# Optimization experiments

Hardware: AMD Instinct MI355X
Metric: run time of the kernel (lower is better)

The kernel has to match this reference:

```python
import jax, jax.numpy as jnp
import numpy as np

H = 8          # heads
D_MODEL = 64   # padded embedding dim (power of 2)
D_K = 8        # per-head dim -> NQ=3 qubits
SEQ = 32
NQ = 3
DIM2 = D_K * D_K  # 2*NQ qubit joint space
W_MUL = float(np.sqrt(2.0) * 5 ** (-0.5))  # PQC he_std * lrmul

# ---- static circuit unitaries (qubit 0 = most significant / leftmost in kron) ----

def _cnot(n, c, t):
    dim = 2 ** n
    P = np.zeros((dim, dim), np.complex64)
    for b in range(dim):
        if (b >> (n - 1 - c)) & 1:
            P[b ^ (1 << (n - 1 - t)), b] = 1.0
        else:
            P[b, b] = 1.0
    return P

def _cnot_ring(n):
    U = np.eye(2 ** n, dtype=np.complex64)
    for t in range(n):
        U = _cnot(n, t, (t + 1) % n) @ U  # later gates multiply on the left
    return U

UC6 = jnp.asarray(_cnot_ring(2 * NQ))  # (64,64) entangling ring used by score + sum circuits
MZ6 = jnp.asarray(((-1.0) ** np.array([bin(i).count('1') for i in range(2 ** (2 * NQ))])).astype(np.complex64))  # Z^{otimes 2n} diagonal

# ---- parameterized single-qubit rotations (batched, differentiable) ----

def _rx(t):
    c = jnp.cos(t / 2).astype(jnp.complex64)
    s = jnp.sin(t / 2).astype(jnp.complex64)
    return jnp.stack([jnp.stack([c, -1j * s], -1), jnp.stack([-1j * s, c], -1)], -2)

def _ry(t):
    c = jnp.cos(t / 2).astype(jnp.complex64)
    s = jnp.sin(t / 2).astype(jnp.complex64)
    return jnp.stack([jnp.stack([c, -s], -1), jnp.stack([s, c], -1)], -2)

def _rz(t):
    e = jnp.exp(-0.5j * t.astype(jnp.complex64))
    z = jnp.zeros_like(e)
    return jnp.stack([jnp.stack([e, z], -1), jnp.stack([z, e.conj()], -1)], -2)

def _kron3(a, b, c):
    out = jnp.einsum('...ad,...be,...cf->...abcdef', a, b, c)
    return out.reshape(out.shape[:-6] + (D_K, D_K))

def _pqc_unitaries(w):
    # w: (H, 3, NQ*3); per qubit apply rx, ry, rz -> per-qubit u = Rz@Ry@Rx, circuit = kron
    a = (w * W_MUL).reshape(H, 3, NQ, 3)
    u = _rz(a[..., 2]) @ _ry(a[..., 1]) @ _rx(a[..., 0])  # (H,3,NQ,2,2)
    return _kron3(u[..., 0, :, :], u[..., 1, :, :], u[..., 2, :, :])  # (H,3,dk,dk)

def _forward(x, pqc_w, W1, b1, W2, b2):
    x = jnp.pad(x, ((0, 0), (0, 0), (0, D_MODEL - x.shape[-1])))
    xq = (x @ W1.T + b1)[0]                                    # (S, d_k) linear1
    psi = xq / jnp.sqrt(jnp.sum(xq * xq, -1, keepdims=True))   # amplitude encoding
    rho = (psi[:, :, None] * psi[:, None, :]).astype(jnp.complex64)  # (S,dk,dk) pure-state density matrices
    Upqc = _pqc_unitaries(pqc_w)                               # (H, 3=[q,k,v], dk, dk)
    rqkv = jnp.einsum('hgab,sbc,hgdc->hgsad', Upqc, rho, Upqc.conj())
    qs, ks_, vs = rqkv[:, 0], rqkv[:, 1], rqkv[:, 2]           # (H,S,dk,dk)
    # score_ij = (Re tr(Z^{2n} U (q_i kron k_j) U^dag) + 1)/2 = (Re tr(A (q kron k)) + 1)/2
    A = (UC6.conj().T * MZ6) @ UC6                             # U^dag Z^{2n} U, (64,64)
    A4 = A.reshape(D_K, D_K, D_K, D_K)                         # [(c,d),(a,b)]
    T = jnp.einsum('cdab,hiac->hidb', A4, qs)
    scores = (jnp.einsum('hidb,hjbd->hij', T, ks_).real + 1.0) * 0.5  # (H,S,S)
    # weighted value: per-qubit rx(phi/2) ry(phi/2) rz(phi) with phi=(score-0.5)*2pi
    phi = (scores - 0.5) * (2.0 * jnp.pi)
    u1 = _rz(phi) @ _ry(phi * 0.5) @ _rx(phi * 0.5)            # (H,S,S,2,2)
    Uw = _kron3(u1, u1, u1)                                    # (H,S,S,dk,dk)
    wvs = Uw @ vs[:, None] @ Uw.conj().swapaxes(-1, -2)        # (H,S_i,S_j,dk,dk)

    def step(rho_a, wv_j):
        # cal_sum fold: kron, entangle with CNOT ring, partial-trace out 2nd register
        rho_ab = jnp.einsum('...ij,...kl->...ikjl', rho_a, wv_j).reshape(H, SEQ, DIM2, DIM2)
        out = UC6 @ rho_ab @ UC6.conj().T
        out = out.reshape(H, SEQ, D_K, D_K, D_K, D_K)
        return jnp.einsum('...abcb->...ac', out), None

    rho_fin, _ = jax.lax.scan(step, wvs[:, :, 0], jnp.moveaxis(wvs[:, :, 1:], 2, 0))
    z = jnp.diagonal(rho_fin, axis1=-2, axis2=-1).real         # (H,S,dk) computational-basis probs
    zs = jnp.transpose(z, (1, 0, 2)).reshape(1, SEQ, H * D_K)  # concat heads
    return zs @ W2.T + b2                                      # linear2; dropout = identity (eval)

def setup_inputs():
    key = jax.random.key(0)
    kk = jax.random.split(key, 4)
    x = jax.random.normal(kk[0], (1, SEQ, D_MODEL), jnp.float32)
    pqc_w = jax.random.uniform(kk[1], (H, 3, NQ * 3), jnp.float32, 0.0, 2.0 * float(np.pi))
    W1 = jax.random.normal(kk[2], (D_K, D_MODEL), jnp.float32) / np.sqrt(D_MODEL).astype(np.float32)
    b1 = jnp.zeros((D_K,), jnp.float32)
    W2 = jax.random.normal(kk[3], (D_MODEL, D_MODEL), jnp.float32) / np.sqrt(D_MODEL).astype(np.float32)
    b2 = jnp.zeros((D_MODEL,), jnp.float32)
    return {"x": x, "pqc_w": pqc_w, "W1": W1, "b1": b1, "W2": W2, "b2": b2, "edge_index": 0}

def reference(x, pqc_w, W1, b1, W2, b2, edge_index):
    # edge_index sentinel 0 == None (dense attention path)
    return _forward(x, pqc_w, W1, b1, W2, b2)
```

## Files before the change

kernel.cpp:

```cpp
#include <hip/hip_runtime.h>

#define NHEAD 8
#define SEQL  32
static constexpr float W_MUL = 0.632455532033675866f;
static constexpr float PI_F  = 3.14159265358979323846f;

__device__ __forceinline__ float2 cmulf(float2 a, float2 b) {
    return make_float2(a.x*b.x - a.y*b.y, a.x*b.y + a.y*b.x);
}
__device__ __forceinline__ float2 caddf(float2 a, float2 b) {
    return make_float2(a.x + b.x, a.y + b.y);
}
__device__ __forceinline__ int sig3(int a) {
    int a2=(a>>2)&1, a1=(a>>1)&1, a0=a&1;
    return (a2<<2) | ((a1^a2)<<1) | (a0^a1);
}

__global__ __launch_bounds__(512) void kfused(const float* __restrict__ x,
                                              const float* __restrict__ pqc_w,
                                              const float* __restrict__ W1,
                                              const float* __restrict__ b1,
                                              const float* __restrict__ W2,
                                              const float* __restrict__ b2,
                                              float* __restrict__ out) {
    __shared__ float  xq[SEQL][8];
    __shared__ float  psi[SEQL][8];
    __shared__ float2 us[NHEAD][9][4];
    __shared__ float2 U8s[NHEAD][3][64];
    __shared__ __align__(16) float2 Carr[NHEAD][SEQL][4][2];
    __shared__ float2 w0s[NHEAD][8];
    __shared__ float  Zs[NHEAD][8];

    const int t = threadIdx.x;
    const int l = t & 63;
    const int h = t >> 6;
    const int i = blockIdx.x;

    if (t < 256) {
        const int s = t >> 3, k = t & 7;
        const float4* xr = (const float4*)(x  + s*64);
        const float4* wr = (const float4*)(W1 + k*64);
        float acc = b1[k];
        #pragma unroll
        for (int q = 0; q < 16; ++q) {
            float4 xa = xr[q], wa = wr[q];
            acc += xa.x*wa.x + xa.y*wa.y + xa.z*wa.z + xa.w*wa.w;
        }
        xq[s][k] = acc;
    }
    if (l < 9) {
        const int g = l / 3, q = l % 3;
        const int base = h*27 + g*9 + q*3;
        float t0 = pqc_w[base+0] * W_MUL;
        float t1 = pqc_w[base+1] * W_MUL;
        float t2 = pqc_w[base+2] * W_MUL;
        float c0, s0, c1, s1, cz, sz;
        sincosf(t0*0.5f, &s0, &c0);
        sincosf(t1*0.5f, &s1, &c1);
        sincosf(t2*0.5f, &sz, &cz);
        float2 m00 = make_float2(c1*c0,  s1*s0);
        float2 m01 = make_float2(-s1*c0, -c1*s0);
        float2 m10 = make_float2(s1*c0,  -c1*s0);
        float2 m11 = make_float2(c1*c0,  -s1*s0);
        float2 em = make_float2(cz, -sz), ep = make_float2(cz, sz);
        us[h][l][0] = cmulf(em, m00);
        us[h][l][1] = cmulf(em, m01);
        us[h][l][2] = cmulf(ep, m10);
        us[h][l][3] = cmulf(ep, m11);
    }
    __syncthreads();

    if (t < 256) {
        const int s = t >> 3, k = t & 7;
        float ss = 0.f;
        #pragma unroll
        for (int kk = 0; kk < 8; ++kk) ss += xq[s][kk]*xq[s][kk];
        psi[s][k] = xq[s][k] * rsqrtf(ss);
    }
    {
        const int r = l >> 3, c = l & 7;
        const int i0 = ((r>>2)<<1)       | (c>>2);
        const int i1 = (((r>>1)&1)<<1)   | ((c>>1)&1);
        const int i2 = ((r&1)<<1)        | (c&1);
        #pragma unroll
        for (int g = 0; g < 3; ++g)
            U8s[h][g][l] = cmulf(cmulf(us[h][g*3+0][i0], us[h][g*3+1][i1]),
                                 us[h][g*3+2][i2]);
    }
    __syncthreads();

    {
        const int j = l >> 1, half = l & 1;

        float qhi = 0.f;
        #pragma unroll
        for (int a = 0; a < 8; ++a) {
            float2 ph = make_float2(0.f, 0.f);
            #pragma unroll
            for (int b = 0; b < 8; ++b) {
                float pb = psi[i][b];
                float2 ue = U8s[h][0][a*8 + b];
                ph.x += ue.x * pb;
                ph.y += ue.y * pb;
            }
            float sign = (((a>>2) ^ a) & 1) ? -1.f : 1.f;
            qhi += sign * (ph.x*ph.x + ph.y*ph.y);
        }
        float kj;
        {
            float acc = 0.f;
            #pragma unroll
            for (int aa = 0; aa < 4; ++aa) {
                int a = half*4 + aa;
                float2 ph = make_float2(0.f, 0.f);
                #pragma unroll
                for (int b = 0; b < 8; ++b) {
                    float pb = psi[j][b];
                    float2 ue = U8s[h][1][a*8 + b];
                    ph.x += ue.x * pb;
                    ph.y += ue.y * pb;
                }
                float sign = ((a>>1) & 1) ? -1.f : 1.f;
                acc += sign * (ph.x*ph.x + ph.y*ph.y);
            }
            kj = acc + __shfl_xor(acc, 1, 64);
        }
        float2 w[8];
        #pragma unroll
        for (int a = 0; a < 8; ++a) {
            float2 ph = make_float2(0.f, 0.f);
            #pragma unroll
            for (int b = 0; b < 8; ++b) {
                float pb = psi[j][b];
                float2 ue = U8s[h][2][a*8 + b];
                ph.x += ue.x * pb;
                ph.y += ue.y * pb;
            }
            w[a] = ph;
        }
        float phi = PI_F * qhi * kj;
        float c1, s1, ch, sh;
        sincosf(phi*0.25f, &s1, &c1);
        sincosf(phi*0.5f,  &sh, &ch);
        float2 em = make_float2(ch, -sh), ep = make_float2(ch, sh);
        float sc = s1*c1;
        float2 u00 = cmulf(em, make_float2(c1*c1,  s1*s1));
        float2 u01 = cmulf(em, make_float2(-sc, -sc));
        float2 u10 = cmulf(ep, make_float2(sc, -sc));
        float2 u11 = cmulf(ep, make_float2(c1*c1, -s1*s1));

        #pragma unroll
        for (int p = 0; p < 4; ++p) {
            float2 lo = w[p], hi = w[p+4];
            w[p]   = caddf(cmulf(u00, lo), cmulf(u01, hi));
            w[p+4] = caddf(cmulf(u10, lo), cmulf(u11, hi));
        }
        #pragma unroll
        for (int p = 0; p < 4; ++p) {
            int i0 = ((p >> 1) << 2) | (p & 1);
            float2 lo = w[i0], hi = w[i0+2];
            w[i0]   = caddf(cmulf(u00, lo), cmulf(u01, hi));
            w[i0+2] = caddf(cmulf(u10, lo), cmulf(u11, hi));
        }
        #pragma unroll
        for (int p = 0; p < 4; ++p) {
            float2 lo = w[2*p], hi = w[2*p+1];
            w[2*p]   = caddf(cmulf(u00, lo), cmulf(u01, hi));
            w[2*p+1] = caddf(cmulf(u10, lo), cmulf(u11, hi));
        }

        if (l == 0) {
            #pragma unroll
            for (int b = 0; b < 8; ++b) w0s[h][b] = w[b];
        }
        const int mset0[4] = {0,3,5,6}, mset1[4] = {1,2,4,7};
        #pragma unroll
        for (int combo = 0; combo < 4; ++combo) {
            int a0 = combo >> 1, c0 = combo & 1;
            float2 acc = make_float2(0.f, 0.f);
            #pragma unroll
            for (int tt = 0; tt < 4; ++tt) {
                int m = half ? mset1[tt] : mset0[tt];
                float2 wx = w[(a0<<2)^m], wy = w[(c0<<2)^m];
                acc.x += wx.x*wy.x + wx.y*wy.y;
                acc.y += wx.y*wy.x - wx.x*wy.y;
            }
            Carr[h][j][combo][half] = acc;
        }
    }
    __syncthreads();

    {
        const int a = l >> 3, c = l & 7;
        const int combo = ((a & 1) << 1) | (c & 1);
        const int src0 = (sig3(a) << 3) | sig3(c);
        const int src1 = src0 ^ 54;

        float2 wa = w0s[h][a], wc = w0s[h][c];
        float rr = wa.x*wc.x + wa.y*wc.y;
        float ri = wa.y*wc.x - wa.x*wc.y;

        for (int j = 1; j < SEQL; ++j) {
            float4 Cv = *((const float4*)&Carr[h][j][combo][0]);
            float R0r = __shfl(rr, src0, 64);
            float R0i = __shfl(ri, src0, 64);
            float R1r = __shfl(rr, src1, 64);
            float R1i = __shfl(ri, src1, 64);
            float nr = Cv.x*R0r - Cv.y*R0i + Cv.z*R1r - Cv.w*R1i;
            float ni = Cv.x*R0i + Cv.y*R0r + Cv.z*R1i + Cv.w*R1r;
            rr = nr; ri = ni;
        }
        if (a == c) Zs[h][a] = rr;
    }
    __syncthreads();

    {
        const int m = t >> 3, p = t & 7;
        float acc = 0.f;
        #pragma unroll
        for (int cc = 0; cc < 8; ++cc)
            acc += Zs[p][cc] * W2[m*64 + p*8 + cc];
        acc += __shfl_xor(acc, 1, 64);
        acc += __shfl_xor(acc, 2, 64);
        acc += __shfl_xor(acc, 4, 64);
        if (p == 0) out[i*64 + m] = acc + b2[m];
    }
}

extern "C" void kernel_launch(void* const* d_in, const int* in_sizes, int n_in,
                              void* d_out, int out_size, void* d_ws, size_t ws_size,
                              hipStream_t stream) {
    const float* x     = (const float*)d_in[0];
    const float* pqc_w = (const float*)d_in[1];
    const float* W1    = (const float*)d_in[2];
    const float* b1    = (const float*)d_in[3];
    const float* W2    = (const float*)d_in[4];
    const float* b2    = (const float*)d_in[5];

    hipLaunchKernelGGL(kfused, dim3(SEQL), dim3(512), 0, stream,
                       x, pqc_w, W1, b1, W2, b2, (float*)d_out);
}
```

Before: 81.28 us.

## Split score/value projections across lane pairs, prefetch W2, use fast trig

The query-score projection, previously computed redundantly by all 32 lanes of each head, now runs only on the lane pair for j==i and is shared through shared memory. Key and value projections are split across the two half-lanes of each pair, with the values written to shared memory and read back after an extra barrier. The W2 and b2 loads are issued at kernel start to hide global-memory latency, linear1 is split across all 512 threads with a shuffle reduction, and sincosf is replaced by __sinf/__cosf. The cost is an additional __syncthreads, more shared memory, and reduced trig accuracy.

```diff
diff --git a/kernel.cpp b/kernel.cpp
--- a/kernel.cpp
+++ b/kernel.cpp
@@ -27,6 +27,9 @@
     __shared__ float  psi[SEQL][8];
     __shared__ float2 us[NHEAD][9][4];
     __shared__ float2 U8s[NHEAD][3][64];
+    __shared__ float  Ks[NHEAD][SEQL];
+    __shared__ float  Qs[NHEAD];
+    __shared__ __align__(16) float2 Vs[NHEAD][SEQL][8];
     __shared__ __align__(16) float2 Carr[NHEAD][SEQL][4][2];
     __shared__ float2 w0s[NHEAD][8];
     __shared__ float  Zs[NHEAD][8];
@@ -36,28 +39,33 @@
     const int h = t >> 6;
     const int i = blockIdx.x;
 
-    if (t < 256) {
-        const int s = t >> 3, k = t & 7;
-        const float4* xr = (const float4*)(x  + s*64);
-        const float4* wr = (const float4*)(W1 + k*64);
-        float acc = b1[k];
-        #pragma unroll
-        for (int q = 0; q < 16; ++q) {
+    const int mE = t >> 3, pE = t & 7;
+    const float4 w2a = *(const float4*)(W2 + mE*64 + pE*8);
+    const float4 w2b = *(const float4*)(W2 + mE*64 + pE*8 + 4);
+    const float  b2m = b2[mE];
+
+    {
+        const int s = t >> 4, k = (t >> 1) & 7, hf = t & 1;
+        const float4* xr = (const float4*)(x  + s*64) + hf*8;
+        const float4* wr = (const float4*)(W1 + k*64) + hf*8;
+        float acc = hf ? 0.f : b1[k];
+        #pragma unroll
+        for (int q = 0; q < 8; ++q) {
             float4 xa = xr[q], wa = wr[q];
             acc += xa.x*wa.x + xa.y*wa.y + xa.z*wa.z + xa.w*wa.w;
         }
-        xq[s][k] = acc;
+        acc += __shfl_xor(acc, 1, 64);
+        if (!hf) xq[s][k] = acc;
     }
     if (l < 9) {
         const int g = l / 3, q = l % 3;
         const int base = h*27 + g*9 + q*3;
-        float t0 = pqc_w[base+0] * W_MUL;
-        float t1 = pqc_w[base+1] * W_MUL;
-        float t2 = pqc_w[base+2] * W_MUL;
-        float c0, s0, c1, s1, cz, sz;
-        sincosf(t0*0.5f, &s0, &c0);
-        sincosf(t1*0.5f, &s1, &c1);
-        sincosf(t2*0.5f, &sz, &cz);
+        float t0 = pqc_w[base+0] * (W_MUL*0.5f);
+        float t1 = pqc_w[base+1] * (W_MUL*0.5f);
+        float t2 = pqc_w[base+2] * (W_MUL*0.5f);
+        float c0 = __cosf(t0), s0 = __sinf(t0);
+        float c1 = __cosf(t1), s1 = __sinf(t1);
+        float cz = __cosf(t2), sz = __sinf(t2);
         float2 m00 = make_float2(c1*c0,  s1*s0);
         float2 m01 = make_float2(-s1*c0, -c1*s0);
         float2 m10 = make_float2(s1*c0,  -c1*s0);
@@ -90,44 +98,27 @@
     __syncthreads();
 
     {
-        const int j = l >> 1, half = l & 1;
-
-        float qhi = 0.f;
-        #pragma unroll
-        for (int a = 0; a < 8; ++a) {
+        const int j = l >> 1, half = l & 1, abase = half << 2;
+        float kacc = 0.f;
+        #pragma unroll
+        for (int aa = 0; aa < 4; ++aa) {
+            int a = abase + aa;
             float2 ph = make_float2(0.f, 0.f);
             #pragma unroll
             for (int b = 0; b < 8; ++b) {
-                float pb = psi[i][b];
-                float2 ue = U8s[h][0][a*8 + b];
+                float pb = psi[j][b];
+                float2 ue = U8s[h][1][a*8 + b];
                 ph.x += ue.x * pb;
                 ph.y += ue.y * pb;
             }
-            float sign = (((a>>2) ^ a) & 1) ? -1.f : 1.f;
-            qhi += sign * (ph.x*ph.x + ph.y*ph.y);
-        }
-        float kj;
-        {
-            float acc = 0.f;
-            #pragma unroll
-            for (int aa = 0; aa < 4; ++aa) {
-                int a = half*4 + aa;
-                float2 ph = make_float2(0.f, 0.f);
-                #pragma unroll
-                for (int b = 0; b < 8; ++b) {
-                    float pb = psi[j][b];
-                    float2 ue = U8s[h][1][a*8 + b];
-                    ph.x += ue.x * pb;
-                    ph.y += ue.y * pb;
-                }
-                float sign = ((a>>1) & 1) ? -1.f : 1.f;
-                acc += sign * (ph.x*ph.x + ph.y*ph.y);
-            }
-            kj = acc + __shfl_xor(acc, 1, 64);
-        }
-        float2 w[8];
-        #pragma unroll
-        for (int a = 0; a < 8; ++a) {
+            float sign = ((a>>1) & 1) ? -1.f : 1.f;
+            kacc += sign * (ph.x*ph.x + ph.y*ph.y);
+        }
+        kacc += __shfl_xor(kacc, 1, 64);
+        if (!half) Ks[h][j] = kacc;
+        #pragma unroll
+        for (int aa = 0; aa < 4; ++aa) {
+            int a = abase + aa;
             float2 ph = make_float2(0.f, 0.f);
             #pragma unroll
             for (int b = 0; b < 8; ++b) {
@@ -136,12 +127,35 @@
                 ph.x += ue.x * pb;
                 ph.y += ue.y * pb;
             }
-            w[a] = ph;
-        }
-        float phi = PI_F * qhi * kj;
-        float c1, s1, ch, sh;
-        sincosf(phi*0.25f, &s1, &c1);
-        sincosf(phi*0.5f,  &sh, &ch);
+            Vs[h][j][a] = ph;
+        }
+        if (j == i) {
+            float qacc = 0.f;
+            #pragma unroll
+            for (int aa = 0; aa < 4; ++aa) {
+                int a = abase + aa;
+                float2 ph = make_float2(0.f, 0.f);
+                #pragma unroll
+                for (int b = 0; b < 8; ++b) {
+                    float pb = psi[i][b];
+                    float2 ue = U8s[h][0][a*8 + b];
+                    ph.x += ue.x * pb;
+                    ph.y += ue.y * pb;
+                }
+                float sign = (((a>>2) ^ a) & 1) ? -1.f : 1.f;
+                qacc += sign * (ph.x*ph.x + ph.y*ph.y);
+            }
+            qacc += __shfl_xor(qacc, 1, 64);
+            if (!half) Qs[h] = qacc;
+        }
+    }
+    __syncthreads();
+
+    {
+        const int j = l >> 1, half = l & 1;
+        const float phi = PI_F * Qs[h] * Ks[h][j];
+        float c1 = __cosf(phi*0.25f), s1 = __sinf(phi*0.25f);
+        float ch = __cosf(phi*0.5f),  sh = __sinf(phi*0.5f);
         float2 em = make_float2(ch, -sh), ep = make_float2(ch, sh);
         float sc = s1*c1;
         float2 u00 = cmulf(em, make_float2(c1*c1,  s1*s1));
@@ -149,6 +163,9 @@
         float2 u10 = cmulf(ep, make_float2(sc, -sc));
         float2 u11 = cmulf(ep, make_float2(c1*c1, -s1*s1));
 
+        float2 w[8];
+        #pragma unroll
+        for (int b = 0; b < 8; ++b) w[b] = Vs[h][j][b];
         #pragma unroll
         for (int p = 0; p < 4; ++p) {
             float2 lo = w[p], hi = w[p+4];
@@ -215,15 +232,14 @@
     __syncthreads();
 
     {
-        const int m = t >> 3, p = t & 7;
-        float acc = 0.f;
-        #pragma unroll
-        for (int cc = 0; cc < 8; ++cc)
-            acc += Zs[p][cc] * W2[m*64 + p*8 + cc];
+        float acc = Zs[pE][0]*w2a.x + Zs[pE][1]*w2a.y
+                  + Zs[pE][2]*w2a.z + Zs[pE][3]*w2a.w
+                  + Zs[pE][4]*w2b.x + Zs[pE][5]*w2b.y
+                  + Zs[pE][6]*w2b.z + Zs[pE][7]*w2b.w;
         acc += __shfl_xor(acc, 1, 64);
         acc += __shfl_xor(acc, 2, 64);
         acc += __shfl_xor(acc, 4, 64);
-        if (p == 0) out[i*64 + m] = acc + b2[m];
+        if (pE == 0) out[i*64 + mE] = acc + b2m;
     }
 }
 
```

New measurement: 79.94 us. No clear change (-1.6%).
